# Kernel tuning notes

Measured on AMD Instinct MI355X. Metric: run time of the kernel, lower is better.

## Reference

```python
import jax, jax.numpy as jnp
import numpy as np

B, N, C = 8, 4096, 768
H, HD = 12, 64          # num_heads, head_dim = C // H
M = HD * 2              # rand_feat_dim
LAM = 0.3
NUM_STEP = 5


def setup_inputs() -> dict:
    key = jax.random.key(0)
    k1, k2, k3, k4 = jax.random.split(key, 4)
    x = jax.random.normal(k1, (B, N, C), dtype=jnp.float32)
    Wqkv = jax.random.normal(k2, (C, 2 * C), dtype=jnp.float32) * 0.02
    Wproj = jax.random.normal(k3, (C, C), dtype=jnp.float32) * 0.02
    bproj = jnp.zeros((C,), dtype=jnp.float32)
    rand_matrix = jax.random.normal(k4, (H, HD, M), dtype=jnp.float32)
    return {"x": x, "Wqkv": Wqkv, "Wproj": Wproj, "bproj": bproj,
            "rand_matrix": rand_matrix}


def _soft(z, t):
    # sign(z) * relu(|z| - t): soft-thresholding (ISTA proximal step)
    return jnp.sign(z) * jax.nn.relu(jnp.abs(z) - t)


def reference(x, Wqkv, Wproj, bproj, rand_matrix):
    Bn, Nn, Cn = x.shape
    Hh, hd, m = rand_matrix.shape
    scale = hd ** (-0.5)

    qkv = x @ Wqkv                                   # [B,N,2C]
    q = qkv[..., :Cn].reshape(Bn, Nn, Hh, hd).transpose(0, 2, 1, 3)  # [B,H,N,hd]
    v = qkv[..., Cn:].reshape(Bn, Nn, Hh, hd).transpose(0, 2, 1, 3)  # [B,H,N,hd]

    # random-feature map: exp(q @ proj - ||q||^2 / 2) / sqrt(m)
    qs = q * scale ** 0.5
    rf = jnp.exp(jnp.einsum('bhnd,hdm->bhnm', qs, rand_matrix)
                 - 0.5 * jnp.sum(qs * qs, axis=-1, keepdims=True)) / m ** 0.5
    # F.normalize(p=2, dim=-2): normalize over the sequence axis
    qn = rf / jnp.maximum(jnp.linalg.norm(rf, axis=-2, keepdims=True), 1e-12)

    kk = jnp.einsum('bhnm,bhnp->bhmp', qn, qn)       # [B,H,m,m]
    kv = jnp.einsum('bhnm,bhnd->bhmd', qn, v)        # [B,H,m,hd]

    # Lipschitz bound: max row L1 norm of kk, detached
    L = jax.lax.stop_gradient(
        jnp.max(jnp.sum(jnp.abs(kk), axis=-1), axis=-1))[..., None, None] + 1.0

    # unrolled ISTA soft-thresholding loop
    s = _soft(kv, LAM)
    for _ in range(NUM_STEP):
        s = _soft(s - (kk @ s - kv) / L, LAM / L)

    out = jnp.einsum('bhnm,bhmd->bhnd', qn, s)       # [B,H,N,hd]
    out = out.transpose(0, 2, 1, 3).reshape(Bn, Nn, Cn)
    return out @ Wproj + bproj
```

## Files before the change

kernel.cpp:

```cpp
#include <hip/hip_runtime.h>


typedef __attribute__((ext_vector_type(8))) short bf16x8;
typedef __attribute__((ext_vector_type(4))) float f32x4;

#define GLD16(gptr, lptr)                                                              \
  __builtin_amdgcn_global_load_lds((const __attribute__((address_space(1))) void*)(gptr), \
                                   (__attribute__((address_space(3))) void*)(lptr), 16, 0, 0)

__device__ __forceinline__ unsigned short f2bf(float f) {
  union { float f; unsigned int u; } v; v.f = f;
  unsigned int r = v.u + 0x7fffu + ((v.u >> 16) & 1u);
  return (unsigned short)(r >> 16);
}
__device__ __forceinline__ float bf2f(unsigned short s) {
  union { unsigned int u; float f; } v; v.u = ((unsigned int)s) << 16;
  return v.f;
}
__device__ __forceinline__ float rn_of(float css) {
  return 1.f / fmaxf(sqrtf(css), 1e-12f);
}

template<int ITERS>
__device__ __forceinline__ void gemm256_core(
    const unsigned short* __restrict__ A,
    const unsigned short* __restrict__ B,
    int ldk,
    f32x4 (&acc)[8][4],
    unsigned short* smem) {
  const int tid = threadIdx.x;
  const int lane = tid & 63, wave = tid >> 6;
  const int l16 = lane & 15, quad = lane >> 4;
  const int wr = wave >> 2, wc = wave & 3;
  const int rsw = l16 & 7;

#pragma unroll
  for (int i = 0; i < 8; i++)
#pragma unroll
    for (int j = 0; j < 4; j++)
#pragma unroll
      for (int r = 0; r < 4; r++) acc[i][j][r] = 0.f;

  const int srow0 = tid >> 3, sc0 = ((tid & 7) ^ (srow0 & 7)) << 3;
  const int srow1 = (tid + 512) >> 3, sc1 = ((tid & 7) ^ (srow1 & 7)) << 3;
  const int dstw = wave * 512;

  auto stageA = [&](int T, int h) {
    const unsigned short* g = A + (long)(h * 128) * ldk + T * 64;
    unsigned short* d = smem + (T & 1) * 32768 + h * 8192 + dstw;
    GLD16(g + (long)srow0 * ldk + sc0, d);
    GLD16(g + (long)srow1 * ldk + sc1, d + 4096);
  };
  auto stageB = [&](int T, int h) {
    const unsigned short* g = B + (long)(h * 128) * ldk + T * 64;
    unsigned short* d = smem + (T & 1) * 32768 + 16384 + h * 8192 + dstw;
    GLD16(g + (long)srow0 * ldk + sc0, d);
    GLD16(g + (long)srow1 * ldk + sc1, d + 4096);
  };

  bf16x8 af[4][2], bn[4][2];

  auto rdA_ks = [&](int b, int mh, int ks) {
    const unsigned short* p = smem + b * 32768 + wr * 8192 + (mh * 64 + l16) * 64;
#pragma unroll
    for (int ii = 0; ii < 4; ii++)
      af[ii][ks] = *(const bf16x8*)(p + ii * 1024 + (((ks * 4 + quad) ^ rsw) << 3));
  };
  auto rdB_ks = [&](int b, int ks) {
    const unsigned short* p = smem + b * 32768 + 16384 + (wc >> 1) * 8192 +
                              ((wc & 1) * 64 + l16) * 64;
#pragma unroll
    for (int jj = 0; jj < 4; jj++)
      bn[jj][ks] = *(const bf16x8*)(p + jj * 1024 + (((ks * 4 + quad) ^ rsw) << 3));
  };

  auto mma16 = [&](int mh, int ks) {
    __builtin_amdgcn_s_setprio(1);
#pragma unroll
    for (int ii = 0; ii < 4; ii++)
#pragma unroll
      for (int jj = 0; jj < 4; jj++)
        acc[mh * 4 + ii][jj] = __builtin_amdgcn_mfma_f32_16x16x32_bf16(
            af[ii][ks], bn[jj][ks], acc[mh * 4 + ii][jj], 0, 0, 0);
    __builtin_amdgcn_s_setprio(0);
  };

#define FENCE asm volatile("" ::: "memory")
#define SGB __builtin_amdgcn_sched_barrier(0)
#define LGKM(n) asm volatile("s_waitcnt lgkmcnt(" #n ")" ::: "memory")

  stageA(0, 0); stageA(0, 1); stageB(0, 0); stageB(0, 1);
  stageB(1, 0); stageB(1, 1);
  asm volatile("s_waitcnt vmcnt(4)" ::: "memory");
  __builtin_amdgcn_s_barrier();

#pragma unroll 1
  for (int i = 0; i < ITERS; i++) {
    const int u = 2 * i;
    const bool more = (i + 1 < ITERS);
    stageA(u + 1, 0);
    rdB_ks(0, 0); rdA_ks(0, 0, 0);
    SGB;
    rdB_ks(0, 1); rdA_ks(0, 0, 1);
    FENCE; __builtin_amdgcn_s_barrier();
    LGKM(8); SGB;
    mma16(0, 0);
    LGKM(0); SGB;
    mma16(0, 1);
    FENCE; __builtin_amdgcn_s_barrier();
    stageA(u + 1, 1);
    if (more) stageB(u + 2, 0);
    rdA_ks(0, 1, 0);
    SGB;
    rdA_ks(0, 1, 1);
    FENCE; __builtin_amdgcn_s_barrier();
    LGKM(4); SGB;
    mma16(1, 0);
    LGKM(0); SGB;
    mma16(1, 1);
    if (more) { asm volatile("s_waitcnt vmcnt(2)" ::: "memory"); }
    else      { asm volatile("s_waitcnt vmcnt(0)" ::: "memory"); }
    FENCE; __builtin_amdgcn_s_barrier();
    if (more) { stageB(u + 2, 1); stageA(u + 2, 0); stageA(u + 2, 1); }
    rdB_ks(1, 0); rdA_ks(1, 0, 0);
    SGB;
    rdB_ks(1, 1); rdA_ks(1, 0, 1);
    FENCE; __builtin_amdgcn_s_barrier();
    LGKM(8); SGB;
    mma16(0, 0);
    LGKM(0); SGB;
    mma16(0, 1);
    FENCE; __builtin_amdgcn_s_barrier();
    if (more) { stageB(u + 3, 0); stageB(u + 3, 1); }
    rdA_ks(1, 1, 0);
    SGB;
    rdA_ks(1, 1, 1);
    FENCE; __builtin_amdgcn_s_barrier();
    LGKM(4); SGB;
    mma16(1, 0);
    LGKM(0); SGB;
    mma16(1, 1);
    if (more) { asm volatile("s_waitcnt vmcnt(4)" ::: "memory"); }
    FENCE; __builtin_amdgcn_s_barrier();
  }
#undef FENCE
#undef SGB
#undef LGKM
}

template<int NT>
__device__ __forceinline__ void gemm128x256_core(
    const unsigned short* __restrict__ A,
    const unsigned short* __restrict__ B,
    int ldk,
    f32x4 (&acc)[4][4],
    unsigned short* smem) {
  const int tid = threadIdx.x;
  const int lane = tid & 63, wave = tid >> 6;
  const int l16 = lane & 15, quad = lane >> 4;
  const int wr = wave >> 2, wc = wave & 3;
  const int rsw = l16 & 7;

#pragma unroll
  for (int m = 0; m < 4; m++)
#pragma unroll
    for (int n = 0; n < 4; n++)
#pragma unroll
      for (int r = 0; r < 4; r++) acc[m][n][r] = 0.f;

  const int srow0 = tid >> 3, sc0 = ((tid & 7) ^ (srow0 & 7)) << 3;
  const int srow1 = (tid + 512) >> 3, sc1 = ((tid & 7) ^ (srow1 & 7)) << 3;
  const int dstw = wave * 512;

  auto stage = [&](int T) {
    unsigned short* d = smem + (T & 1) * 24576;
    const unsigned short* gA = A + T * 64;
    const unsigned short* gB = B + T * 64;
    GLD16(gA + (long)srow0 * ldk + sc0, d + dstw);
    GLD16(gA + (long)srow1 * ldk + sc1, d + 4096 + dstw);
    GLD16(gB + (long)srow0 * ldk + sc0, d + 8192 + dstw);
    GLD16(gB + (long)srow1 * ldk + sc1, d + 8192 + 4096 + dstw);
    GLD16(gB + (long)(srow0 + 128) * ldk + sc0, d + 16384 + dstw);
    GLD16(gB + (long)(srow1 + 128) * ldk + sc1, d + 16384 + 4096 + dstw);
  };

  bf16x8 af[4][2], bn[4][2];

  auto rdA_ks = [&](int b, int ks) {
    const unsigned short* p = smem + b * 24576 + (wr * 64 + l16) * 64;
#pragma unroll
    for (int m = 0; m < 4; m++)
      af[m][ks] = *(const bf16x8*)(p + m * 1024 + (((ks * 4 + quad) ^ rsw) << 3));
  };
  auto rdB_ks = [&](int b, int ks) {
    const unsigned short* p = smem + b * 24576 + 8192 + (wc * 64 + l16) * 64;
#pragma unroll
    for (int n = 0; n < 4; n++)
      bn[n][ks] = *(const bf16x8*)(p + n * 1024 + (((ks * 4 + quad) ^ rsw) << 3));
  };

  auto mma16 = [&](int ks) {
    __builtin_amdgcn_s_setprio(1);
#pragma unroll
    for (int m = 0; m < 4; m++)
#pragma unroll
      for (int n = 0; n < 4; n++)
        acc[m][n] = __builtin_amdgcn_mfma_f32_16x16x32_bf16(
            af[m][ks], bn[n][ks], acc[m][n], 0, 0, 0);
    __builtin_amdgcn_s_setprio(0);
  };

#define FENCE asm volatile("" ::: "memory")
#define SGB __builtin_amdgcn_sched_barrier(0)
#define LGKM(n) asm volatile("s_waitcnt lgkmcnt(" #n ")" ::: "memory")

  stage(0); stage(1);
  asm volatile("s_waitcnt vmcnt(6)" ::: "memory");
  __builtin_amdgcn_s_barrier();

#pragma unroll 1
  for (int t = 0; t < NT; t++) {
    const int b = t & 1;
    rdA_ks(b, 0); rdB_ks(b, 0);
    SGB;
    rdA_ks(b, 1); rdB_ks(b, 1);
    LGKM(8); SGB;
    mma16(0);
    LGKM(0); SGB;
    mma16(1);
    FENCE; __builtin_amdgcn_s_barrier();
    if (t + 2 < NT) stage(t + 2);
    if (t + 1 < NT) {
      if (t + 2 < NT) { asm volatile("s_waitcnt vmcnt(6)" ::: "memory"); }
      else            { asm volatile("s_waitcnt vmcnt(0)" ::: "memory"); }
      FENCE; __builtin_amdgcn_s_barrier();
    }
  }
#undef FENCE
#undef SGB
#undef LGKM
}

__global__ __launch_bounds__(256) void k_pre(const float* __restrict__ x,
                                             unsigned short* __restrict__ xbf,
                                             const float* __restrict__ Wqkv,
                                             unsigned short* __restrict__ wqkvT,
                                             const float* __restrict__ Wproj,
                                             unsigned short* __restrict__ wprojT,
                                             const float* __restrict__ rm,
                                             unsigned short* __restrict__ rmT,
                                             float* __restrict__ colss) {
  __shared__ float t[32][33];
  const int bid = blockIdx.x, tid = threadIdx.x;
  if (bid < 24576) {
    long i = (long)bid * 256 + tid;
    float4 v = ((const float4*)x)[i];
    unsigned short o[4] = {f2bf(v.x), f2bf(v.y), f2bf(v.z), f2bf(v.w)};
    ((uint2*)xbf)[i] = *(uint2*)o;
    return;
  }
  int b2 = bid - 24576;
  const float* in; unsigned short* out; int R, C, c0, r0; float scale;
  if (b2 < 1152) {
    in = Wqkv; out = wqkvT; R = 768; C = 1536;
    c0 = (b2 % 48) * 32; r0 = (b2 / 48) * 32; scale = 1.f;
  } else if (b2 < 1152 + 576) {
    b2 -= 1152;
    in = Wproj; out = wprojT; R = 768; C = 768;
    c0 = (b2 % 24) * 32; r0 = (b2 / 24) * 32; scale = 1.f;
  } else if (b2 < 1152 + 576 + 96) {
    b2 -= 1152 + 576;
    int z = b2 / 8;
    in = rm + (long)z * 8192; out = rmT + (long)z * 8192;
    R = 64; C = 128;
    c0 = (b2 % 4) * 32; r0 = ((b2 / 4) & 1) * 32;
    scale = 0.3535533905932738f;
  } else {
    b2 -= 1152 + 576 + 96;
    colss[b2 * 256 + tid] = 0.f;
    return;
  }
  int tx = tid & 31, ty = tid >> 5;
#pragma unroll
  for (int k = 0; k < 32; k += 8)
    t[ty + k][tx] = in[(long)(r0 + ty + k) * C + c0 + tx];
  __syncthreads();
#pragma unroll
  for (int k = 0; k < 32; k += 8)
    out[(long)(c0 + ty + k) * R + r0 + tx] = f2bf(t[tx][ty + k] * scale);
}

__global__ __launch_bounds__(512, 2) void k_gemm_qkv256(const unsigned short* __restrict__ xbf,
                                                        const unsigned short* __restrict__ wqkvT,
                                                        unsigned short* __restrict__ q,
                                                        unsigned short* __restrict__ vT) {
  __shared__ __align__(16) unsigned short smem[65536];
  f32x4 acc[8][4];
  const int L = blockIdx.x;
  const int xcd = L & 7, slot = L >> 3;
  const int rt = xcd * 16 + slot / 6;
  const int ct = slot % 6;
  gemm256_core<6>(xbf + (long)rt * 256 * 768, wqkvT + (long)ct * 256 * 768, 768, acc, smem);

  const int tid = threadIdx.x, lane = tid & 63, wave = tid >> 6;
  const int l16 = lane & 15, quad = lane >> 4;
  const int wr = wave >> 2, wc = wave & 3;
  const int b = rt >> 4;
  const int nbase = (rt & 15) * 256;
  if (ct < 3) {
#pragma unroll
    for (int i = 0; i < 8; i++)
#pragma unroll
      for (int j = 0; j < 4; j++) {
        int col = ct * 256 + wc * 64 + j * 16 + l16;
        int h = col >> 6, d = col & 63;
#pragma unroll
        for (int r = 0; r < 4; r++) {
          int n = nbase + wr * 128 + i * 16 + quad * 4 + r;
          q[((long)(b * 12 + h) * 4096 + n) * 64 + d] = f2bf(acc[i][j][r]);
        }
      }
  } else {
    unsigned short* pool = smem;
    for (int hh = 0; hh < 2; hh++) {
      __syncthreads();
      if (wr == hh) {
#pragma unroll
        for (int i = 0; i < 8; i++)
#pragma unroll
          for (int j = 0; j < 4; j++)
#pragma unroll
            for (int r = 0; r < 4; r++)
              pool[(wc * 64 + j * 16 + l16) * 136 + i * 16 + quad * 4 + r] = f2bf(acc[i][j][r]);
      }
      __syncthreads();
#pragma unroll
      for (int it = 0; it < 8; it++) {
        int chunk = it * 512 + tid;
        int col = chunk >> 4, ng = chunk & 15;
        uint4 val = *(const uint4*)&pool[col * 136 + ng * 8];
        int vcol = (ct - 3) * 256 + col;
        int h = vcol >> 6, d = vcol & 63;
        long n = nbase + hh * 128 + ng * 8;
        *(uint4*)&vT[((long)(b * 12 + h) * 64 + d) * 4096 + n] = val;
      }
    }
  }
}

__global__ __launch_bounds__(256) void k_gemm_rf(const unsigned short* __restrict__ q,
                                                 const unsigned short* __restrict__ rmT,
                                                 unsigned short* __restrict__ qnT,
                                                 float* __restrict__ colss) {
  __shared__ __align__(16) unsigned short smem[16384];
  __shared__ float hnp[256];
  __shared__ float css[128];
  unsigned short* Asm = smem;
  unsigned short* Bsm = smem + 8192;
  unsigned short* pool = smem;
  f32x4 acc[4][4];
  const int nt = blockIdx.x, bh = blockIdx.y, h = bh % 12;
  const int tid = threadIdx.x, lane = tid & 63, wave = tid >> 6;
  const int l16 = lane & 15, quad = lane >> 4;
  const int wm = (wave >> 1) * 64, wn = (wave & 1) * 64;
  const int fsw = (l16 >> 1) & 3;
  const unsigned short* Aq = q + ((long)bh * 4096 + nt * 128) * 64;
  const unsigned short* Brm = rmT + (long)h * 8192;

#pragma unroll
  for (int c = 0; c < 4; c++) {
    int chunk = c * 256 + tid;
    int row = chunk >> 3, ko8 = chunk & 7;
    int kc = ko8 >> 2;
    int c2s = (ko8 & 3) ^ ((row >> 1) & 3);
    *(uint4*)(Asm + kc * 4096 + row * 32 + c2s * 8) = *(const uint4*)(Aq + (long)row * 64 + ko8 * 8);
    *(uint4*)(Bsm + kc * 4096 + row * 32 + c2s * 8) = *(const uint4*)(Brm + (long)row * 64 + ko8 * 8);
  }
  for (int i = tid; i < 128; i += 256) css[i] = 0.f;
  __syncthreads();
  {
    const unsigned short* ap = Asm + (tid & 1) * 4096 + (tid >> 1) * 32;
    float ssum = 0.f;
#pragma unroll
    for (int e = 0; e < 32; e++) { float f = bf2f(ap[e]); ssum += f * f; }
    hnp[tid] = ssum;
  }
#pragma unroll
  for (int i = 0; i < 4; i++)
#pragma unroll
    for (int j = 0; j < 4; j++)
#pragma unroll
      for (int r = 0; r < 4; r++) acc[i][j][r] = 0.f;
#pragma unroll
  for (int kc = 0; kc < 2; kc++) {
    bf16x8 af[4], bfr[4];
#pragma unroll
    for (int i = 0; i < 4; i++)
      af[i] = *(const bf16x8*)(Asm + kc * 4096 + (wm + i * 16 + l16) * 32 + ((quad ^ fsw) * 8));
#pragma unroll
    for (int j = 0; j < 4; j++)
      bfr[j] = *(const bf16x8*)(Bsm + kc * 4096 + (wn + j * 16 + l16) * 32 + ((quad ^ fsw) * 8));
#pragma unroll
    for (int i = 0; i < 4; i++)
#pragma unroll
      for (int j = 0; j < 4; j++)
        acc[i][j] = __builtin_amdgcn_mfma_f32_16x16x32_bf16(af[i], bfr[j], acc[i][j], 0, 0, 0);
  }
  __syncthreads();
  float hnv[4][4];
#pragma unroll
  for (int i = 0; i < 4; i++)
#pragma unroll
    for (int r = 0; r < 4; r++) {
      int row = wm + i * 16 + quad * 4 + r;
      hnv[i][r] = 0.0625f * (hnp[2 * row] + hnp[2 * row + 1]);
    }
#pragma unroll
  for (int j = 0; j < 4; j++) {
    int col = wn + j * 16 + l16;
    float cp = 0.f;
#pragma unroll
    for (int i = 0; i < 4; i++)
#pragma unroll
      for (int r = 0; r < 4; r++) {
        float v = __expf(acc[i][j][r] - hnv[i][r]) * 0.08838834764831845f;
        acc[i][j][r] = v;
        cp += v * v;
      }
    atomicAdd(&css[col], cp);
  }
  __syncthreads();
  for (int i = tid; i < 128; i += 256) atomicAdd(&colss[bh * 128 + i], css[i]);
  for (int hh = 0; hh < 2; hh++) {
    __syncthreads();
    if ((wave >> 1) == hh) {
#pragma unroll
      for (int i = 0; i < 4; i++)
#pragma unroll
        for (int j = 0; j < 4; j++)
#pragma unroll
          for (int r = 0; r < 4; r++)
            pool[(i * 16 + quad * 4 + r) * 134 + wn + j * 16 + l16] = f2bf(acc[i][j][r]);
    }
    __syncthreads();
#pragma unroll
    for (int c = 0; c < 4; c++) {
      int chunk = tid + c * 256;
      int m = chunk >> 3, nj = (chunk & 7) * 8;
      unsigned short o[8];
#pragma unroll
      for (int e = 0; e < 8; e++) o[e] = pool[(nj + e) * 134 + m];
      *(uint4*)&qnT[((long)bh * 128 + m) * 4096 + nt * 128 + hh * 64 + nj] = *(uint4*)o;
    }
  }
}

__global__ __launch_bounds__(256) void k_gemm_kkkv(const unsigned short* __restrict__ qnT,
                                                   const unsigned short* __restrict__ vT,
                                                   const float* __restrict__ colss,
                                                   unsigned short* __restrict__ kkp) {
  __shared__ __align__(16) unsigned short As[128 * 32], Bs[64 * 32];
  f32x4 acc[4][6];
  const int ks = blockIdx.x, bh = blockIdx.y;
  const unsigned short* A = qnT + (long)bh * 128 * 4096 + ks * 512;
  const unsigned short* B1 = vT + (long)bh * 64 * 4096 + ks * 512;
  const int tid = threadIdx.x, lane = tid & 63, wave = tid >> 6;
  const int l16 = lane & 15, quad = lane >> 4;
  const int wm = (wave >> 1) * 64, wn = (wave & 1) * 96;
  const int arow = tid >> 2;
  const int akos = (((tid & 3) ^ ((arow >> 1) & 3)) << 3);
  const int fsw = (l16 >> 1) & 3;
#pragma unroll
  for (int i = 0; i < 4; i++)
#pragma unroll
    for (int j = 0; j < 6; j++)
#pragma unroll
      for (int r = 0; r < 4; r++) acc[i][j][r] = 0.f;
  for (int k0 = 0; k0 < 512; k0 += 32) {
    __syncthreads();
    GLD16(A + (long)arow * 4096 + k0 + akos, As + wave * 512);
    GLD16(A + (long)(arow + 64) * 4096 + k0 + akos, As + 2048 + wave * 512);
    GLD16(B1 + (long)arow * 4096 + k0 + akos, Bs + wave * 512);
    __syncthreads();
    bf16x8 af[4], bfr[6];
#pragma unroll
    for (int i = 0; i < 4; i++)
      af[i] = *(const bf16x8*)(As + (wm + i * 16 + l16) * 32 + ((quad ^ fsw) * 8));
#pragma unroll
    for (int j = 0; j < 6; j++) {
      int row = wn + j * 16 + l16;
      const unsigned short* rp = (row < 128) ? (As + row * 32) : (Bs + (row - 128) * 32);
      bfr[j] = *(const bf16x8*)(rp + ((quad ^ fsw) * 8));
    }
#pragma unroll
    for (int i = 0; i < 4; i++)
#pragma unroll
      for (int j = 0; j < 6; j++)
        acc[i][j] = __builtin_amdgcn_mfma_f32_16x16x32_bf16(af[i], bfr[j], acc[i][j], 0, 0, 0);
  }
  unsigned short* dst = kkp + ((long)ks * 96 + bh) * 24576;
  float rnr[4][4];
#pragma unroll
  for (int i = 0; i < 4; i++)
#pragma unroll
    for (int r = 0; r < 4; r++)
      rnr[i][r] = rn_of(colss[bh * 128 + wm + i * 16 + quad * 4 + r]);
#pragma unroll
  for (int j = 0; j < 6; j++) {
    int col = wn + j * 16 + l16;
    float rnc = (col < 128) ? rn_of(colss[bh * 128 + col]) : 1.f;
#pragma unroll
    for (int i = 0; i < 4; i++)
#pragma unroll
      for (int r = 0; r < 4; r++) {
        int row = wm + i * 16 + quad * 4 + r;
        dst[row * 192 + col] = f2bf(acc[i][j][r] * rnr[i][r] * rnc);
      }
  }
}

__global__ __launch_bounds__(256) void k_red(const unsigned short* __restrict__ kkp,
                                             unsigned short* __restrict__ kkred,
                                             float* __restrict__ kvred) {
  const int g = blockIdx.x, bh = blockIdx.y;
  const int tid = threadIdx.x;
  const unsigned short* base = kkp + (long)bh * 24576 + (long)(g * 32) * 192;
#pragma unroll
  for (int c = 0; c < 3; c++) {
    int idx = c * 256 + tid;
    int m = idx / 24, c8 = idx % 24;
    float f[8] = {0.f, 0.f, 0.f, 0.f, 0.f, 0.f, 0.f, 0.f};
#pragma unroll
    for (int ks = 0; ks < 8; ks++) {
      union { uint4 u; unsigned short s[8]; } u;
      u.u = *(const uint4*)(base + (long)ks * 2359296 + m * 192 + c8 * 8);
#pragma unroll
      for (int e = 0; e < 8; e++) f[e] += bf2f(u.s[e]);
    }
    long row = (long)bh * 128 + g * 32 + m;
    if (c8 < 16) {
      unsigned short o[8];
#pragma unroll
      for (int e = 0; e < 8; e++) o[e] = f2bf(f[e]);
      *(uint4*)&kkred[row * 128 + c8 * 8] = *(uint4*)o;
    } else {
      *(float4*)&kvred[row * 64 + (c8 - 16) * 8] = make_float4(f[0], f[1], f[2], f[3]);
      *(float4*)&kvred[row * 64 + (c8 - 16) * 8 + 4] = make_float4(f[4], f[5], f[6], f[7]);
    }
  }
}

__global__ __launch_bounds__(256) void k_ista2(const unsigned short* __restrict__ kkred,
                                               const float* __restrict__ kvred,
                                               const float* __restrict__ colss,
                                               unsigned short* __restrict__ sT) {
  __shared__ __align__(16) unsigned short kks[128 * 144];
  __shared__ __align__(16) unsigned short ssT[32 * 144];
  __shared__ float kvs[128 * 32];
  __shared__ float red[128];
  __shared__ float rns[128];
  const int tid = threadIdx.x, lane = tid & 63, wave = tid >> 6;
  const int l16 = lane & 15, quad = lane >> 4;
  const int wm = (wave >> 1) * 64, wn = (wave & 1) * 16;
  const int bh = blockIdx.x >> 1, d0 = (blockIdx.x & 1) * 32;
  for (int idx = tid; idx < 2048; idx += 256) {
    int m = idx >> 4, c8 = idx & 15;
    uint4 v = *(const uint4*)(kkred + ((long)bh * 128 + m) * 128 + c8 * 8);
    *(uint4*)&kks[m * 144 + c8 * 8] = v;
  }
  for (int idx = tid; idx < 1024; idx += 256) {
    int m = idx >> 3, c4 = idx & 7;
    float4 v = *(const float4*)(kvred + ((long)bh * 128 + m) * 64 + d0 + c4 * 4);
    *(float4*)&kvs[m * 32 + c4 * 4] = v;
  }
  __syncthreads();
  float kv[4][4];
#pragma unroll
  for (int i = 0; i < 4; i++)
#pragma unroll
    for (int r = 0; r < 4; r++) {
      int m = wm + i * 16 + quad * 4 + r, dl = wn + l16;
      kv[i][r] = kvs[m * 32 + dl];
    }
  if (tid < 128) {
    float rs = 0.f;
    const unsigned short* rp = kks + tid * 144;
    for (int p = 0; p < 128; p++) rs += fabsf(bf2f(rp[p]));
    red[tid] = rs;
    rns[tid] = rn_of(colss[bh * 128 + tid]);
  }
  __syncthreads();
  for (int o = 64; o > 0; o >>= 1) {
    if (tid < o) red[tid] = fmaxf(red[tid], red[tid + o]);
    __syncthreads();
  }
  const float L = red[0] + 1.f;
  const float invL = 1.f / L;
  const float lamL = 0.3f * invL;
  float sreg[4][4];
#pragma unroll
  for (int i = 0; i < 4; i++)
#pragma unroll
    for (int r = 0; r < 4; r++) {
      float z = kv[i][r];
      float az = fabsf(z) - 0.3f;
      float s = az > 0.f ? copysignf(az, z) : 0.f;
      sreg[i][r] = s;
      ssT[(wn + l16) * 144 + wm + i * 16 + quad * 4 + r] = f2bf(s);
    }
  for (int step = 0; step < 5; step++) {
    __syncthreads();
    f32x4 acc[4];
#pragma unroll
    for (int i = 0; i < 4; i++)
#pragma unroll
      for (int r = 0; r < 4; r++) acc[i][r] = 0.f;
#pragma unroll
    for (int kc = 0; kc < 4; kc++) {
      bf16x8 af[4], bfj;
#pragma unroll
      for (int i = 0; i < 4; i++)
        af[i] = *(const bf16x8*)(kks + (wm + i * 16 + l16) * 144 + kc * 32 + quad * 8);
      bfj = *(const bf16x8*)(ssT + (wn + l16) * 144 + kc * 32 + quad * 8);
#pragma unroll
      for (int i = 0; i < 4; i++)
        acc[i] = __builtin_amdgcn_mfma_f32_16x16x32_bf16(af[i], bfj, acc[i], 0, 0, 0);
    }
    __syncthreads();
#pragma unroll
    for (int i = 0; i < 4; i++)
#pragma unroll
      for (int r = 0; r < 4; r++) {
        float z = sreg[i][r] - (acc[i][r] - kv[i][r]) * invL;
        float az = fabsf(z) - lamL;
        float s = az > 0.f ? copysignf(az, z) : 0.f;
        sreg[i][r] = s;
        ssT[(wn + l16) * 144 + wm + i * 16 + quad * 4 + r] = f2bf(s);
      }
  }
#pragma unroll
  for (int i = 0; i < 4; i++)
#pragma unroll
    for (int r = 0; r < 4; r++) {
      int m = wm + i * 16 + quad * 4 + r, d = d0 + wn + l16;
      sT[(long)bh * 8192 + d * 128 + m] = f2bf(sreg[i][r] * rns[m]);
    }
}

__global__ __launch_bounds__(256) void k_gemm_attn(const unsigned short* __restrict__ qnT,
                                                   const unsigned short* __restrict__ sT,
                                                   unsigned short* __restrict__ attn) {
  __shared__ __align__(16) unsigned short As2[4352];
  __shared__ __align__(16) unsigned short Bs[64 * 32];
  f32x4 acc[4][2];
  const int nt = blockIdx.x, bh = blockIdx.y;
  const int b = bh / 12, h = bh % 12;
  const int tid = threadIdx.x, lane = tid & 63, wave = tid >> 6;
  const int l16 = lane & 15, quad = lane >> 4;
  const int wm = (wave >> 1) * 64, wn = (wave & 1) * 32;
  const int fsw = (l16 >> 1) & 3;
#pragma unroll
  for (int i = 0; i < 4; i++)
#pragma unroll
    for (int j = 0; j < 2; j++)
#pragma unroll
      for (int r = 0; r < 4; r++) acc[i][j][r] = 0.f;
  for (int k0 = 0; k0 < 128; k0 += 32) {
    __syncthreads();
#pragma unroll
    for (int it = 0; it < 3; it++) {
      if (it < 2 || tid < 32) {
        int c = it * 256 + tid;
        int p = (c * 241) >> 12;
        int nh = c - p * 17;
        int k = ((p & 7) << 2) + (p >> 3);
        int n8 = (nh < 16 ? nh : 15) << 3;
        const unsigned short* gp = qnT + ((long)bh * 128 + k0 + k) * 4096 + nt * 128 + n8;
        GLD16(gp, As2 + (it * 256 + wave * 64) * 8);
      }
    }
    {
      int dd = tid >> 2;
      int ko = (((tid & 3) ^ ((dd >> 1) & 3)) * 8);
      const unsigned short* gp = sT + ((long)bh * 64 + dd) * 128 + k0 + ko;
      GLD16(gp, Bs + wave * 512);
    }
    __syncthreads();
    bf16x8 af[4], bfr[2];
#pragma unroll
    for (int i = 0; i < 4; i++) {
      union { bf16x8 v; unsigned short s[8]; } u;
#pragma unroll
      for (int e = 0; e < 8; e++) {
        int p = ((e & 3) << 3) + (quad << 1) + (e >> 2);
        u.s[e] = As2[p * 136 + wm + i * 16 + l16];
      }
      af[i] = u.v;
    }
#pragma unroll
    for (int j = 0; j < 2; j++)
      bfr[j] = *(const bf16x8*)&Bs[(wn + j * 16 + l16) * 32 + ((quad ^ fsw) * 8)];
#pragma unroll
    for (int i = 0; i < 4; i++)
#pragma unroll
      for (int j = 0; j < 2; j++)
        acc[i][j] = __builtin_amdgcn_mfma_f32_16x16x32_bf16(af[i], bfr[j], acc[i][j], 0, 0, 0);
  }
#pragma unroll
  for (int i = 0; i < 4; i++)
#pragma unroll
    for (int j = 0; j < 2; j++)
#pragma unroll
      for (int r = 0; r < 4; r++) {
        int n = nt * 128 + wm + i * 16 + quad * 4 + r;
        int dd = wn + j * 16 + l16;
        attn[((long)b * 4096 + n) * 768 + h * 64 + dd] = f2bf(acc[i][j][r]);
      }
}

__global__ __launch_bounds__(512, 2) void k_gemm_proj128(const unsigned short* __restrict__ attn,
                                                         const unsigned short* __restrict__ wprojT,
                                                         const float* __restrict__ bias,
                                                         float* __restrict__ out) {
  __shared__ __align__(16) unsigned short smem[49152];
  f32x4 acc[4][4];
  const int L = blockIdx.x;
  const int xcd = L & 7, slot = L >> 3;
  const int rt = xcd * 32 + slot / 3;
  const int ct = slot % 3;
  gemm128x256_core<12>(attn + (long)rt * 128 * 768, wprojT + (long)ct * 256 * 768, 768,
                       acc, smem);
  const int tid = threadIdx.x, lane = tid & 63, wave = tid >> 6;
  const int l16 = lane & 15, quad = lane >> 4;
  const int wr = wave >> 2, wc = wave & 3;
  const long row0 = (long)rt * 128 + wr * 64;
#pragma unroll
  for (int m = 0; m < 4; m++)
#pragma unroll
    for (int n = 0; n < 4; n++) {
      int col = ct * 256 + wc * 64 + n * 16 + l16;
      float bv = bias[col];
#pragma unroll
      for (int r = 0; r < 4; r++) {
        long row = row0 + m * 16 + quad * 4 + r;
        out[row * 768 + col] = acc[m][n][r] + bv;
      }
    }
}

extern "C" void kernel_launch(void* const* d_in, const int* in_sizes, int n_in,
                              void* d_out, int out_size, void* d_ws, size_t ws_size,
                              hipStream_t stream) {
  const float* x = (const float*)d_in[0];
  const float* Wqkv = (const float*)d_in[1];
  const float* Wproj = (const float*)d_in[2];
  const float* bproj = (const float*)d_in[3];
  const float* rm = (const float*)d_in[4];
  float* out = (float*)d_out;

  size_t o = 0;
  char* wsb = (char*)d_ws;
  auto take = [&](size_t b) { char* p = wsb + o; o += b; return p; };
  unsigned short* wqkvT = (unsigned short*)take(2359296);
  unsigned short* wprojT = (unsigned short*)take(1179648);
  unsigned short* rmT = (unsigned short*)take(196608);
  unsigned short* q = (unsigned short*)take(50331648);
  unsigned short* vT = (unsigned short*)take(50331648);
  float* colss = (float*)take(49152);
  unsigned short* sT = (unsigned short*)take(1572864);
  if (ws_size < o) return;

  unsigned short* xbf = (unsigned short*)d_out;
  unsigned short* qnT = (unsigned short*)d_out;
  unsigned short* kkp = q;
  unsigned short* attnbf = q;
  unsigned short* kkred = vT;
  float* kvred = (float*)(vT + 1572864);

  k_pre<<<26448, 256, 0, stream>>>(x, xbf, Wqkv, wqkvT, Wproj, wprojT, rm, rmT, colss);
  k_gemm_qkv256<<<768, 512, 0, stream>>>(xbf, wqkvT, q, vT);
  k_gemm_rf<<<dim3(32, 96), 256, 0, stream>>>(q, rmT, qnT, colss);
  k_gemm_kkkv<<<dim3(8, 96), 256, 0, stream>>>(qnT, vT, colss, kkp);
  k_red<<<dim3(4, 96), 256, 0, stream>>>(kkp, kkred, kvred);
  k_ista2<<<192, 256, 0, stream>>>(kkred, kvred, colss, sT);
  k_gemm_attn<<<dim3(32, 96), 256, 0, stream>>>(qnT, sT, attnbf);
  k_gemm_proj128<<<768, 512, 0, stream>>>(attnbf, wprojT, bproj, out);
}
```

Baseline: 441.7 us.

## Double-buffer kk/kv GEMM loads and preload full K in attention GEMM

```diff
diff --git a/kernel.cpp b/kernel.cpp
--- a/kernel.cpp
+++ b/kernel.cpp
@@ -459,7 +459,7 @@
                                                    const unsigned short* __restrict__ vT,
                                                    const float* __restrict__ colss,
                                                    unsigned short* __restrict__ kkp) {
-  __shared__ __align__(16) unsigned short As[128 * 32], Bs[64 * 32];
+  __shared__ __align__(16) unsigned short sm[12288];
   f32x4 acc[4][6];
   const int ks = blockIdx.x, bh = blockIdx.y;
   const unsigned short* A = qnT + (long)bh * 128 * 4096 + ks * 512;
@@ -476,12 +476,22 @@
     for (int j = 0; j < 6; j++)
 #pragma unroll
       for (int r = 0; r < 4; r++) acc[i][j][r] = 0.f;
-  for (int k0 = 0; k0 < 512; k0 += 32) {
-    __syncthreads();
-    GLD16(A + (long)arow * 4096 + k0 + akos, As + wave * 512);
-    GLD16(A + (long)(arow + 64) * 4096 + k0 + akos, As + 2048 + wave * 512);
-    GLD16(B1 + (long)arow * 4096 + k0 + akos, Bs + wave * 512);
-    __syncthreads();
+
+  auto stage = [&](int t) {
+    unsigned short* d = sm + (t & 1) * 6144;
+    GLD16(A + (long)arow * 4096 + t * 32 + akos, d + wave * 512);
+    GLD16(A + (long)(arow + 64) * 4096 + t * 32 + akos, d + 2048 + wave * 512);
+    GLD16(B1 + (long)arow * 4096 + t * 32 + akos, d + 4096 + wave * 512);
+  };
+
+  stage(0); stage(1);
+  asm volatile("s_waitcnt vmcnt(3)" ::: "memory");
+  __builtin_amdgcn_s_barrier();
+
+#pragma unroll 1
+  for (int t = 0; t < 16; t++) {
+    const unsigned short* As = sm + (t & 1) * 6144;
+    const unsigned short* Bs = As + 4096;
     bf16x8 af[4], bfr[6];
 #pragma unroll
     for (int i = 0; i < 4; i++)
@@ -492,12 +502,26 @@
       const unsigned short* rp = (row < 128) ? (As + row * 32) : (Bs + (row - 128) * 32);
       bfr[j] = *(const bf16x8*)(rp + ((quad ^ fsw) * 8));
     }
+    asm volatile("s_waitcnt lgkmcnt(0)" ::: "memory");
+    __builtin_amdgcn_sched_barrier(0);
+    __builtin_amdgcn_s_setprio(1);
 #pragma unroll
     for (int i = 0; i < 4; i++)
 #pragma unroll
       for (int j = 0; j < 6; j++)
         acc[i][j] = __builtin_amdgcn_mfma_f32_16x16x32_bf16(af[i], bfr[j], acc[i][j], 0, 0, 0);
-  }
+    __builtin_amdgcn_s_setprio(0);
+    asm volatile("" ::: "memory");
+    __builtin_amdgcn_s_barrier();
+    if (t + 2 < 16) stage(t + 2);
+    if (t + 1 < 16) {
+      if (t + 2 < 16) { asm volatile("s_waitcnt vmcnt(3)" ::: "memory"); }
+      else            { asm volatile("s_waitcnt vmcnt(0)" ::: "memory"); }
+      asm volatile("" ::: "memory");
+      __builtin_amdgcn_s_barrier();
+    }
+  }
+
   unsigned short* dst = kkp + ((long)ks * 96 + bh) * 24576;
   float rnr[4][4];
 #pragma unroll
@@ -650,8 +674,8 @@
 __global__ __launch_bounds__(256) void k_gemm_attn(const unsigned short* __restrict__ qnT,
                                                    const unsigned short* __restrict__ sT,
                                                    unsigned short* __restrict__ attn) {
-  __shared__ __align__(16) unsigned short As2[4352];
-  __shared__ __align__(16) unsigned short Bs[64 * 32];
+  __shared__ __align__(16) unsigned short As2[17408];
+  __shared__ __align__(16) unsigned short Bs[8192];
   f32x4 acc[4][2];
   const int nt = blockIdx.x, bh = blockIdx.y;
   const int b = bh / 12, h = bh % 12;
@@ -665,27 +689,34 @@
     for (int j = 0; j < 2; j++)
 #pragma unroll
       for (int r = 0; r < 4; r++) acc[i][j][r] = 0.f;
-  for (int k0 = 0; k0 < 128; k0 += 32) {
-    __syncthreads();
-#pragma unroll
-    for (int it = 0; it < 3; it++) {
-      if (it < 2 || tid < 32) {
-        int c = it * 256 + tid;
-        int p = (c * 241) >> 12;
-        int nh = c - p * 17;
-        int k = ((p & 7) << 2) + (p >> 3);
-        int n8 = (nh < 16 ? nh : 15) << 3;
-        const unsigned short* gp = qnT + ((long)bh * 128 + k0 + k) * 4096 + nt * 128 + n8;
-        GLD16(gp, As2 + (it * 256 + wave * 64) * 8);
-      }
-    }
-    {
-      int dd = tid >> 2;
-      int ko = (((tid & 3) ^ ((dd >> 1) & 3)) * 8);
-      const unsigned short* gp = sT + ((long)bh * 64 + dd) * 128 + k0 + ko;
-      GLD16(gp, Bs + wave * 512);
-    }
-    __syncthreads();
+
+#pragma unroll
+  for (int it = 0; it < 9; it++) {
+    if (it < 8 || tid < 128) {
+      int c = it * 256 + tid;
+      int rt_ = (c * 241) >> 12;
+      int nh = c - rt_ * 17;
+      int kc = rt_ >> 5, p = rt_ & 31;
+      int k = kc * 32 + ((p & 7) << 2) + (p >> 3);
+      int n8 = (nh < 16 ? nh : 15) << 3;
+      const unsigned short* gp = qnT + ((long)bh * 128 + k) * 4096 + nt * 128 + n8;
+      GLD16(gp, As2 + c * 8);
+    }
+  }
+#pragma unroll
+  for (int it = 0; it < 4; it++) {
+    int c = it * 256 + tid;
+    int kcp = c >> 8, c8 = c & 255;
+    int dd = c8 >> 2, sub = c8 & 3;
+    int ko = kcp * 32 + ((sub ^ ((dd >> 1) & 3)) << 3);
+    const unsigned short* gp = sT + ((long)bh * 64 + dd) * 128 + ko;
+    GLD16(gp, Bs + c * 8);
+  }
+  asm volatile("s_waitcnt vmcnt(0)" ::: "memory");
+  __builtin_amdgcn_s_barrier();
+
+#pragma unroll
+  for (int kc = 0; kc < 4; kc++) {
     bf16x8 af[4], bfr[2];
 #pragma unroll
     for (int i = 0; i < 4; i++) {
@@ -693,13 +724,13 @@
 #pragma unroll
       for (int e = 0; e < 8; e++) {
         int p = ((e & 3) << 3) + (quad << 1) + (e >> 2);
-        u.s[e] = As2[p * 136 + wm + i * 16 + l16];
+        u.s[e] = As2[(kc * 32 + p) * 136 + wm + i * 16 + l16];
       }
       af[i] = u.v;
     }
 #pragma unroll
     for (int j = 0; j < 2; j++)
-      bfr[j] = *(const bf16x8*)&Bs[(wn + j * 16 + l16) * 32 + ((quad ^ fsw) * 8)];
+      bfr[j] = *(const bf16x8*)&Bs[kc * 2048 + (wn + j * 16 + l16) * 32 + ((quad ^ fsw) * 8)];
 #pragma unroll
     for (int i = 0; i < 4; i++)
 #pragma unroll
```

Result: no change. 442.3 us (+0.1%).
